# Optimization experiments

Measured on AMD Instinct MI355X. Metric: run time of the kernel, lower is better.

The kernel has to match this reference:

```python
import jax, jax.numpy as jnp
import numpy as np

N_NODES = 100000
N_EDGES = 1600000
INPUT_DIM = 128
HIDDEN = 128
OUTPUT_DIM = 2
NUM_LAYERS = 2
MAX_RECURSION = 10
TAU_THRESHOLD = 0.005


def setup_inputs() -> dict:
    key = jax.random.key(0)
    ks = jax.random.split(key, 16)
    s = 0.05
    x = jax.random.normal(ks[0], (N_NODES, INPUT_DIM), dtype=jnp.float32)
    edge_index = jax.random.randint(ks[1], (2, N_EDGES), 0, N_NODES, dtype=jnp.int64)
    W_in = jax.random.normal(ks[2], (HIDDEN, INPUT_DIM), dtype=jnp.float32) * s
    b_in = jax.random.normal(ks[3], (HIDDEN,), dtype=jnp.float32) * s
    Wd = jax.random.normal(ks[4], (NUM_LAYERS, HIDDEN, 2 * HIDDEN), dtype=jnp.float32) * s
    bd = jax.random.normal(ks[5], (NUM_LAYERS, HIDDEN), dtype=jnp.float32) * s
    Wt = jax.random.normal(ks[6], (1, HIDDEN), dtype=jnp.float32) * s
    bt = jax.random.normal(ks[7], (1,), dtype=jnp.float32) * s
    W_ih = jax.random.normal(ks[8], (3 * HIDDEN, HIDDEN), dtype=jnp.float32) * s
    W_hh = jax.random.normal(ks[9], (3 * HIDDEN, HIDDEN), dtype=jnp.float32) * s
    b_ih = jax.random.normal(ks[10], (3 * HIDDEN,), dtype=jnp.float32) * s
    b_hh = jax.random.normal(ks[11], (3 * HIDDEN,), dtype=jnp.float32) * s
    Wo = jax.random.normal(ks[12], (OUTPUT_DIM, HIDDEN), dtype=jnp.float32) * s
    bo = jax.random.normal(ks[13], (OUTPUT_DIM,), dtype=jnp.float32) * s
    return dict(x=x, edge_index=edge_index, W_in=W_in, b_in=b_in, Wd=Wd, bd=bd,
                Wt=Wt, bt=bt, W_ih=W_ih, W_hh=W_hh, b_ih=b_ih, b_hh=b_hh, Wo=Wo, bo=bo)


def _gru_cell(x, h, W_ih, W_hh, b_ih, b_hh):
    # torch.nn.GRUCell math
    gi = x @ W_ih.T + b_ih  # [N, 3H]
    gh = h @ W_hh.T + b_hh
    i_r, i_z, i_n = jnp.split(gi, 3, axis=-1)
    h_r, h_z, h_n = jnp.split(gh, 3, axis=-1)
    r = jax.nn.sigmoid(i_r + h_r)
    z = jax.nn.sigmoid(i_z + h_z)
    n = jnp.tanh(i_n + r * h_n)
    return (1.0 - z) * n + z * h


def reference(x, edge_index, W_in, b_in, Wd, bd, Wt, bt, W_ih, W_hh, b_ih, b_hh, Wo, bo):
    N = x.shape[0]
    row, col = edge_index[0], edge_index[1]
    h = jax.nn.relu(x @ W_in.T + b_in)  # [N, H]
    tau = None
    for l in range(NUM_LAYERS):
        diff = jnp.abs(h[row] - h[col])  # [E, H]
        diff_agg = jax.ops.segment_sum(diff, row, num_segments=N)  # [N, H]
        h = jax.nn.relu(jnp.concatenate([h, diff_agg], axis=-1) @ Wd[l].T + bd[l])
        tau = jax.nn.softplus(h @ Wt.T + bt).squeeze(-1)  # [N]
        # n_updates = clamp(floor(1/tau), max=MAX_RECURSION); node updated iff
        # n_updates > 0 and tau < TAU_THRESHOLD. The original inner loop applies
        # gru(diff_agg[i], h[i]) with the ORIGINAL h[i] each iteration, so repeated
        # application is idempotent -> single masked GRU step is exact same math.
        n_updates = jnp.minimum(jnp.floor(1.0 / tau).astype(jnp.int32), MAX_RECURSION)
        mask = (n_updates > 0) & (tau < TAU_THRESHOLD)
        h_gru = _gru_cell(diff_agg, h, W_ih, W_hh, b_ih, b_hh)
        h = jnp.where(mask[:, None], h_gru, h)
    out = h @ Wo.T + bo  # [N, OUTPUT_DIM]
    return out, tau
```

## Files before the change

kernel.cpp:

```cpp
#include <hip/hip_runtime.h>
#include <cstdint>
#include <cstddef>

#define HID 128
#define BSHIFT 7
#define NSB 256
#define MAXB 4096


__global__ __launch_bounds__(256)
void ecount_kernel(const int* __restrict__ row, int* __restrict__ countsT,
                   int E, int nbuck,
                   const float* __restrict__ W_in, const float* __restrict__ Wd,
                   const float* __restrict__ W_ih, const float* __restrict__ W_hh,
                   float* __restrict__ WinT, float* __restrict__ WdT0,
                   float* __restrict__ WdT1, float* __restrict__ WihT,
                   float* __restrict__ WhhT) {
  for (int i = blockIdx.x * 256 + threadIdx.x; i < 180224; i += NSB * 256) {
    int j = i;
    if (j < 16384) { int r = j >> 7, c = j & 127; WinT[c * 128 + r] = W_in[j]; continue; }
    j -= 16384;
    if (j < 32768) { int r = j >> 8, c = j & 255; WdT0[c * 128 + r] = Wd[j]; continue; }
    j -= 32768;
    if (j < 32768) { int r = j >> 8, c = j & 255; WdT1[c * 128 + r] = Wd[32768 + j]; continue; }
    j -= 32768;
    if (j < 49152) { int r = j >> 7, c = j & 127; WihT[c * 384 + r] = W_ih[j]; continue; }
    j -= 49152;
    { int r = j >> 7, c = j & 127; WhhT[c * 384 + r] = W_hh[j]; }
  }
  __shared__ int lh[1024];
  int b = blockIdx.x;
  for (int i = threadIdx.x; i < nbuck; i += 256) lh[i] = 0;
  __syncthreads();
  int per = (E + NSB - 1) / NSB;
  int s = b * per, e = min(s + per, E);
  for (int i = s + (int)threadIdx.x; i < e; i += 256)
    atomicAdd(&lh[row[i] >> BSHIFT], 1);
  __syncthreads();
  for (int i = threadIdx.x; i < nbuck; i += 256) countsT[i * NSB + b] = lh[i];
}

__global__ __launch_bounds__(NSB)
void bprefix_kernel(int* __restrict__ countsT, int* __restrict__ btotal, int nbuck) {
  __shared__ int sd[NSB];
  int bk = blockIdx.x;
  int t = threadIdx.x;
  int v = countsT[bk * NSB + t];
  sd[t] = v;
  __syncthreads();
  for (int off = 1; off < NSB; off <<= 1) {
    int u = (t >= off) ? sd[t - off] : 0;
    __syncthreads();
    sd[t] += u;
    __syncthreads();
  }
  countsT[bk * NSB + t] = sd[t] - v;
  if (t == NSB - 1) btotal[bk] = sd[t];
}

__global__ __launch_bounds__(1024)
void bstart_kernel(const int* __restrict__ btotal, int* __restrict__ bstart,
                   int* __restrict__ offsets, int N, int nbuck) {
  __shared__ int sd[1024];
  int t = threadIdx.x;
  int v = (t < nbuck) ? btotal[t] : 0;
  sd[t] = v;
  __syncthreads();
  for (int off = 1; off < 1024; off <<= 1) {
    int u = (t >= off) ? sd[t - off] : 0;
    __syncthreads();
    sd[t] += u;
    __syncthreads();
  }
  if (t < nbuck) bstart[t] = sd[t] - v;
  if (t == nbuck - 1) { bstart[nbuck] = sd[t]; offsets[N] = sd[t]; }
}

__global__ __launch_bounds__(256)
void escatter_kernel(const int* __restrict__ row, const int* __restrict__ col,
                     const int* __restrict__ countsT, const int* __restrict__ bstart,
                     int2* __restrict__ ebuf, int E, int nbuck) {
  __shared__ int lcur[1024];
  int b = blockIdx.x;
  for (int i = threadIdx.x; i < nbuck; i += 256)
    lcur[i] = bstart[i] + countsT[i * NSB + b];
  __syncthreads();
  int per = (E + NSB - 1) / NSB;
  int s = b * per, e = min(s + per, E);
  for (int i = s + (int)threadIdx.x; i < e; i += 256) {
    int r = row[i], c = col[i];
    int pos = atomicAdd(&lcur[r >> BSHIFT], 1);
    ebuf[pos] = make_int2(r, c);
  }
}

__global__ __launch_bounds__(256, 6)
void bsort_gin_kernel(const int2* __restrict__ ebuf, const int* __restrict__ bstart,
                      int* __restrict__ offsets, int* __restrict__ csr_col,
                      int N, int nbuck,
                      const float* __restrict__ A, const float* __restrict__ BT,
                      const float* __restrict__ bias, float* __restrict__ C, int G) {
  __shared__ union {
    struct { int cnt[128]; int off[128]; int cur[128]; int lcol[MAXB]; } s;
    struct { float As[32][68]; float Bs[32][128]; } g;
  } sm;
  int bid = blockIdx.x;
  int tid = threadIdx.x;
  if (bid < nbuck) {
    int bk = bid;
    int s = bstart[bk], e = bstart[bk + 1];
    int m = e - s;
    if (tid < 128) sm.s.cnt[tid] = 0;
    __syncthreads();
    for (int i = s + tid; i < e; i += 256)
      atomicAdd(&sm.s.cnt[ebuf[i].x & 127], 1);
    __syncthreads();
    if (tid < 128) sm.s.off[tid] = sm.s.cnt[tid];
    __syncthreads();
    for (int d = 1; d < 128; d <<= 1) {
      int v = 0;
      if (tid < 128 && tid >= d) v = sm.s.off[tid - d];
      __syncthreads();
      if (tid < 128) sm.s.off[tid] += v;
      __syncthreads();
    }
    if (tid < 128) {
      sm.s.cur[tid] = sm.s.off[tid] - sm.s.cnt[tid];
      int node = (bk << BSHIFT) + tid;
      if (node < N) offsets[node] = s + sm.s.off[tid] - sm.s.cnt[tid];
    }
    __syncthreads();
    if (m <= MAXB) {
      for (int i = s + tid; i < e; i += 256) {
        int2 rc = ebuf[i];
        int pos = atomicAdd(&sm.s.cur[rc.x & 127], 1);
        sm.s.lcol[pos] = rc.y;
      }
      __syncthreads();
      if (tid < 128) {
        int b0 = sm.s.off[tid] - sm.s.cnt[tid], b1 = sm.s.off[tid];
        for (int i = b0 + 1; i < b1; ++i) {
          int key = sm.s.lcol[i];
          int j = i - 1;
          while (j >= b0 && sm.s.lcol[j] > key) { sm.s.lcol[j + 1] = sm.s.lcol[j]; --j; }
          sm.s.lcol[j + 1] = key;
        }
      }
      __syncthreads();
      for (int i = tid; i < m; i += 256) csr_col[s + i] = sm.s.lcol[i];
    } else {
      for (int i = s + tid; i < e; i += 256) {
        int2 rc = ebuf[i];
        int pos = atomicAdd(&sm.s.cur[rc.x & 127], 1);
        csr_col[s + pos] = rc.y;
      }
    }
    return;
  }
  int tile = bid - nbuck;
  if (tile >= G) return;
  int tx = tid & 31;
  int ty = tid >> 5;
  int i0 = tile * 64;
  int M = N;
  float acc[8][4] = {};
  for (int kc = 0; kc < 4; ++kc) {
    int ksrc = kc * 32;
    #pragma unroll
    for (int q = 0; q < 2; ++q) {
      int f = q * 256 + tid;
      int i = f >> 3;
      int kq = (f & 7) << 2;
      int ig = i0 + i; if (ig >= M) ig = M - 1;
      float4 v = *(const float4*)(A + (size_t)ig * HID + ksrc + kq);
      sm.g.As[kq + 0][i] = v.x; sm.g.As[kq + 1][i] = v.y;
      sm.g.As[kq + 2][i] = v.z; sm.g.As[kq + 3][i] = v.w;
    }
    #pragma unroll
    for (int q = 0; q < 4; ++q) {
      int f = q * 256 + tid;
      int k = f >> 5; int c4 = (f & 31) << 2;
      *(float4*)&sm.g.Bs[k][c4] = *(const float4*)(BT + (size_t)(ksrc + k) * HID + c4);
    }
    __syncthreads();
    #pragma unroll
    for (int k = 0; k < 32; ++k) {
      float a[8];
      const float4* ap = (const float4*)&sm.g.As[k][ty * 8];
      float4 a0 = ap[0], a1 = ap[1];
      a[0]=a0.x; a[1]=a0.y; a[2]=a0.z; a[3]=a0.w;
      a[4]=a1.x; a[5]=a1.y; a[6]=a1.z; a[7]=a1.w;
      float4 b4 = *(const float4*)&sm.g.Bs[k][tx * 4];
      #pragma unroll
      for (int r = 0; r < 8; ++r) {
        acc[r][0] = fmaf(a[r], b4.x, acc[r][0]);
        acc[r][1] = fmaf(a[r], b4.y, acc[r][1]);
        acc[r][2] = fmaf(a[r], b4.z, acc[r][2]);
        acc[r][3] = fmaf(a[r], b4.w, acc[r][3]);
      }
    }
    __syncthreads();
  }
  float4 bias4 = *(const float4*)(bias + tx * 4);
  #pragma unroll
  for (int r = 0; r < 8; ++r) {
    int row = i0 + ty * 8 + r;
    if (row >= M) continue;
    float4 v4 = make_float4(fmaxf(acc[r][0] + bias4.x, 0.f),
                            fmaxf(acc[r][1] + bias4.y, 0.f),
                            fmaxf(acc[r][2] + bias4.z, 0.f),
                            fmaxf(acc[r][3] + bias4.w, 0.f));
    *(float4*)(C + (size_t)row * HID + tx * 4) = v4;
  }
}

__device__ __forceinline__ void agg_one_node(const float* __restrict__ h,
                                             const int* __restrict__ offsets,
                                             const int* __restrict__ csr_col,
                                             float* __restrict__ diff, int node) {
  int lane = threadIdx.x & 63;
  int start = offsets[node], end = offsets[node + 1];
  int deg = end - start;
  const float2* hrow = (const float2*)(h + (size_t)node * HID);
  float2 hv = hrow[lane];
  float a0 = 0.f, a1 = 0.f;

  int batch = min(deg, 64);
  int myc = (lane < batch) ? csr_col[start + lane] : 0;
  int j = 0;
  for (; j + 16 <= batch; j += 16) {
    const float2* p0 = (const float2*)(h + (size_t)__shfl(myc, j + 0) * HID);
    const float2* p1 = (const float2*)(h + (size_t)__shfl(myc, j + 1) * HID);
    const float2* p2 = (const float2*)(h + (size_t)__shfl(myc, j + 2) * HID);
    const float2* p3 = (const float2*)(h + (size_t)__shfl(myc, j + 3) * HID);
    const float2* p4 = (const float2*)(h + (size_t)__shfl(myc, j + 4) * HID);
    const float2* p5 = (const float2*)(h + (size_t)__shfl(myc, j + 5) * HID);
    const float2* p6 = (const float2*)(h + (size_t)__shfl(myc, j + 6) * HID);
    const float2* p7 = (const float2*)(h + (size_t)__shfl(myc, j + 7) * HID);
    const float2* q0 = (const float2*)(h + (size_t)__shfl(myc, j + 8) * HID);
    const float2* q1 = (const float2*)(h + (size_t)__shfl(myc, j + 9) * HID);
    const float2* q2 = (const float2*)(h + (size_t)__shfl(myc, j + 10) * HID);
    const float2* q3 = (const float2*)(h + (size_t)__shfl(myc, j + 11) * HID);
    const float2* q4 = (const float2*)(h + (size_t)__shfl(myc, j + 12) * HID);
    const float2* q5 = (const float2*)(h + (size_t)__shfl(myc, j + 13) * HID);
    const float2* q6 = (const float2*)(h + (size_t)__shfl(myc, j + 14) * HID);
    const float2* q7 = (const float2*)(h + (size_t)__shfl(myc, j + 15) * HID);
    float2 x0 = p0[lane], x1 = p1[lane], x2 = p2[lane], x3 = p3[lane];
    float2 x4 = p4[lane], x5 = p5[lane], x6 = p6[lane], x7 = p7[lane];
    float2 y0 = q0[lane], y1 = q1[lane], y2 = q2[lane], y3 = q3[lane];
    float2 y4 = q4[lane], y5 = q5[lane], y6 = q6[lane], y7 = q7[lane];
    a0 += fabsf(hv.x - x0.x) + fabsf(hv.x - x1.x) + fabsf(hv.x - x2.x) + fabsf(hv.x - x3.x)
        + fabsf(hv.x - x4.x) + fabsf(hv.x - x5.x) + fabsf(hv.x - x6.x) + fabsf(hv.x - x7.x);
    a1 += fabsf(hv.y - x0.y) + fabsf(hv.y - x1.y) + fabsf(hv.y - x2.y) + fabsf(hv.y - x3.y)
        + fabsf(hv.y - x4.y) + fabsf(hv.y - x5.y) + fabsf(hv.y - x6.y) + fabsf(hv.y - x7.y);
    a0 += fabsf(hv.x - y0.x) + fabsf(hv.x - y1.x) + fabsf(hv.x - y2.x) + fabsf(hv.x - y3.x)
        + fabsf(hv.x - y4.x) + fabsf(hv.x - y5.x) + fabsf(hv.x - y6.x) + fabsf(hv.x - y7.x);
    a1 += fabsf(hv.y - y0.y) + fabsf(hv.y - y1.y) + fabsf(hv.y - y2.y) + fabsf(hv.y - y3.y)
        + fabsf(hv.y - y4.y) + fabsf(hv.y - y5.y) + fabsf(hv.y - y6.y) + fabsf(hv.y - y7.y);
  }
  for (; j + 8 <= batch; j += 8) {
    const float2* p0 = (const float2*)(h + (size_t)__shfl(myc, j + 0) * HID);
    const float2* p1 = (const float2*)(h + (size_t)__shfl(myc, j + 1) * HID);
    const float2* p2 = (const float2*)(h + (size_t)__shfl(myc, j + 2) * HID);
    const float2* p3 = (const float2*)(h + (size_t)__shfl(myc, j + 3) * HID);
    const float2* p4 = (const float2*)(h + (size_t)__shfl(myc, j + 4) * HID);
    const float2* p5 = (const float2*)(h + (size_t)__shfl(myc, j + 5) * HID);
    const float2* p6 = (const float2*)(h + (size_t)__shfl(myc, j + 6) * HID);
    const float2* p7 = (const float2*)(h + (size_t)__shfl(myc, j + 7) * HID);
    float2 x0 = p0[lane], x1 = p1[lane], x2 = p2[lane], x3 = p3[lane];
    float2 x4 = p4[lane], x5 = p5[lane], x6 = p6[lane], x7 = p7[lane];
    a0 += fabsf(hv.x - x0.x) + fabsf(hv.x - x1.x) + fabsf(hv.x - x2.x) + fabsf(hv.x - x3.x)
        + fabsf(hv.x - x4.x) + fabsf(hv.x - x5.x) + fabsf(hv.x - x6.x) + fabsf(hv.x - x7.x);
    a1 += fabsf(hv.y - x0.y) + fabsf(hv.y - x1.y) + fabsf(hv.y - x2.y) + fabsf(hv.y - x3.y)
        + fabsf(hv.y - x4.y) + fabsf(hv.y - x5.y) + fabsf(hv.y - x6.y) + fabsf(hv.y - x7.y);
  }
  for (; j < batch; ++j) {
    const float2* p = (const float2*)(h + (size_t)__shfl(myc, j) * HID);
    float2 x = p[lane];
    a0 += fabsf(hv.x - x.x);
    a1 += fabsf(hv.y - x.y);
  }
  for (int e = start + 64; e < end; ++e) {
    const float2* p = (const float2*)(h + (size_t)csr_col[e] * HID);
    float2 x = p[lane];
    a0 += fabsf(hv.x - x.x);
    a1 += fabsf(hv.y - x.y);
  }
  *(float2*)(diff + (size_t)node * HID + 2 * lane) = make_float2(a0, a1);
}

__global__ __launch_bounds__(256, 6)
void fused_ap1_kernel(const float* __restrict__ h, const int* __restrict__ offsets,
                      const int* __restrict__ csr_col, float* __restrict__ diff,
                      const float* __restrict__ BT, float* __restrict__ Cpart,
                      int M, int G) {
  __shared__ float As[32][68];
  __shared__ float Bs[32][128];
  int bid = blockIdx.x;
  int tid = threadIdx.x;
  int q17 = bid / 17, r17 = bid % 17;
  if (r17 == 0 && q17 < G) {
    int tx = tid & 31;
    int ty = tid >> 5;
    int i0 = q17 * 64;
    float acc[8][4] = {};
    for (int kc = 0; kc < 4; ++kc) {
      int ksrc = kc * 32;
      #pragma unroll
      for (int q = 0; q < 2; ++q) {
        int f = q * 256 + tid;
        int i = f >> 3;
        int kq = (f & 7) << 2;
        int ig = i0 + i; if (ig >= M) ig = M - 1;
        float4 v = *(const float4*)(h + (size_t)ig * HID + ksrc + kq);
        As[kq + 0][i] = v.x; As[kq + 1][i] = v.y;
        As[kq + 2][i] = v.z; As[kq + 3][i] = v.w;
      }
      #pragma unroll
      for (int q = 0; q < 4; ++q) {
        int f = q * 256 + tid;
        int k = f >> 5; int c4 = (f & 31) << 2;
        *(float4*)&Bs[k][c4] = *(const float4*)(BT + (size_t)(ksrc + k) * HID + c4);
      }
      __syncthreads();
      #pragma unroll
      for (int k = 0; k < 32; ++k) {
        float a[8];
        const float4* ap = (const float4*)&As[k][ty * 8];
        float4 a0 = ap[0], a1 = ap[1];
        a[0]=a0.x; a[1]=a0.y; a[2]=a0.z; a[3]=a0.w;
        a[4]=a1.x; a[5]=a1.y; a[6]=a1.z; a[7]=a1.w;
        float4 b4 = *(const float4*)&Bs[k][tx * 4];
        #pragma unroll
        for (int r = 0; r < 8; ++r) {
          acc[r][0] = fmaf(a[r], b4.x, acc[r][0]);
          acc[r][1] = fmaf(a[r], b4.y, acc[r][1]);
          acc[r][2] = fmaf(a[r], b4.z, acc[r][2]);
          acc[r][3] = fmaf(a[r], b4.w, acc[r][3]);
        }
      }
      __syncthreads();
    }
    #pragma unroll
    for (int r = 0; r < 8; ++r) {
      int row = i0 + ty * 8 + r;
      if (row < M) {
        *(float4*)(Cpart + (size_t)row * HID + tx * 4) =
            make_float4(acc[r][0], acc[r][1], acc[r][2], acc[r][3]);
      }
    }
  } else {
    int ngemm_before = (bid + 16) / 17; if (ngemm_before > G) ngemm_before = G;
    int aidx = bid - ngemm_before;
    int wave = tid >> 6;
    int node = aidx * 4 + wave;
    if (node >= M) return;
    agg_one_node(h, offsets, csr_col, diff, node);
  }
}

template<bool OUT>
__global__ __launch_bounds__(256)
void gemm_p2_kernel(const float* __restrict__ A2, const float* __restrict__ BT,
                    const float* __restrict__ bias, float* __restrict__ C,
                    int M,
                    const float* __restrict__ Wt, const float* __restrict__ bt,
                    float* __restrict__ tau_out,
                    const float* __restrict__ WihT, const float* __restrict__ WhhT,
                    const float* __restrict__ b_ih, const float* __restrict__ b_hh,
                    const float* __restrict__ Wo, const float* __restrict__ bo,
                    float* __restrict__ outp) {
  __shared__ float As[32][68];
  __shared__ float Bs[32][128];
  __shared__ float taured[64];
  __shared__ float dl_s[HID];
  __shared__ float hl_s[HID];
  __shared__ int mrows[64];
  __shared__ int mcnt_s;
  __shared__ float osum_s[2][2];
  int tid = threadIdx.x;
  int tx = tid & 31;
  int ty = tid >> 5;
  int i0 = blockIdx.x * 64;
  if (tid == 0) mcnt_s = 0;
  float acc[8][4] = {};
  #pragma unroll
  for (int r = 0; r < 8; ++r) {
    int row = i0 + ty * 8 + r;
    if (row < M) {
      float4 v = *(const float4*)(C + (size_t)row * HID + tx * 4);
      acc[r][0] = v.x; acc[r][1] = v.y; acc[r][2] = v.z; acc[r][3] = v.w;
    }
  }
  for (int kc = 4; kc < 8; ++kc) {
    int ksrc = (kc & 3) * 32;
    int kglob = kc * 32;
    #pragma unroll
    for (int q = 0; q < 2; ++q) {
      int f = q * 256 + tid;
      int i = f >> 3;
      int kq = (f & 7) << 2;
      int ig = i0 + i; if (ig >= M) ig = M - 1;
      float4 v = *(const float4*)(A2 + (size_t)ig * HID + ksrc + kq);
      As[kq + 0][i] = v.x; As[kq + 1][i] = v.y;
      As[kq + 2][i] = v.z; As[kq + 3][i] = v.w;
    }
    #pragma unroll
    for (int q = 0; q < 4; ++q) {
      int f = q * 256 + tid;
      int k = f >> 5; int c4 = (f & 31) << 2;
      *(float4*)&Bs[k][c4] = *(const float4*)(BT + (size_t)(kglob + k) * HID + c4);
    }
    __syncthreads();
    #pragma unroll
    for (int k = 0; k < 32; ++k) {
      float a[8];
      const float4* ap = (const float4*)&As[k][ty * 8];
      float4 a0 = ap[0], a1 = ap[1];
      a[0]=a0.x; a[1]=a0.y; a[2]=a0.z; a[3]=a0.w;
      a[4]=a1.x; a[5]=a1.y; a[6]=a1.z; a[7]=a1.w;
      float4 b4 = *(const float4*)&Bs[k][tx * 4];
      #pragma unroll
      for (int r = 0; r < 8; ++r) {
        acc[r][0] = fmaf(a[r], b4.x, acc[r][0]);
        acc[r][1] = fmaf(a[r], b4.y, acc[r][1]);
        acc[r][2] = fmaf(a[r], b4.z, acc[r][2]);
        acc[r][3] = fmaf(a[r], b4.w, acc[r][3]);
      }
    }
    __syncthreads();
  }

  float4 bias4 = *(const float4*)(bias + tx * 4);
  float bias_r[4] = {bias4.x, bias4.y, bias4.z, bias4.w};
  float4 w4 = *(const float4*)(Wt + tx * 4);
  float wt_r[4] = {w4.x, w4.y, w4.z, w4.w};
  float4 wo0 = make_float4(0.f, 0.f, 0.f, 0.f);
  float4 wo1 = make_float4(0.f, 0.f, 0.f, 0.f);
  if constexpr (OUT) {
    wo0 = *(const float4*)(Wo + tx * 4);
    wo1 = *(const float4*)(Wo + 128 + tx * 4);
  }
  #pragma unroll
  for (int r = 0; r < 8; ++r) {
    int row = i0 + ty * 8 + r;
    bool ok = row < M;
    float v0 = fmaxf(acc[r][0] + bias_r[0], 0.f);
    float v1 = fmaxf(acc[r][1] + bias_r[1], 0.f);
    float v2 = fmaxf(acc[r][2] + bias_r[2], 0.f);
    float v3 = fmaxf(acc[r][3] + bias_r[3], 0.f);
    if (ok) {
      float4 v4 = make_float4(v0, v1, v2, v3);
      *(float4*)(C + (size_t)row * HID + tx * 4) = v4;
    }
    if constexpr (OUT) {
      float o0 = v0 * wo0.x + v1 * wo0.y + v2 * wo0.z + v3 * wo0.w;
      float o1 = v0 * wo1.x + v1 * wo1.y + v2 * wo1.z + v3 * wo1.w;
      o0 += __shfl_down(o0, 16, 32); o1 += __shfl_down(o1, 16, 32);
      o0 += __shfl_down(o0, 8, 32);  o1 += __shfl_down(o1, 8, 32);
      o0 += __shfl_down(o0, 4, 32);  o1 += __shfl_down(o1, 4, 32);
      o0 += __shfl_down(o0, 2, 32);  o1 += __shfl_down(o1, 2, 32);
      o0 += __shfl_down(o0, 1, 32);  o1 += __shfl_down(o1, 1, 32);
      if (tx == 0 && ok) {
        outp[(size_t)row * 2 + 0] = o0 + bo[0];
        outp[(size_t)row * 2 + 1] = o1 + bo[1];
      }
    }
    {
      float pf = v0 * wt_r[0];
      pf = fmaf(v1, wt_r[1], pf);
      pf = fmaf(v2, wt_r[2], pf);
      pf = fmaf(v3, wt_r[3], pf);
      pf += __shfl_down(pf, 16, 32);
      pf += __shfl_down(pf, 8, 32);
      pf += __shfl_down(pf, 4, 32);
      pf += __shfl_down(pf, 2, 32);
      pf += __shfl_down(pf, 1, 32);
      if (tx == 0) taured[ty * 8 + r] = pf;
    }
  }
  __syncthreads();
  if (tid < 64) {
    int row = i0 + tid;
    if (row < M) {
      float pre = taured[tid] + bt[0];
      float tau = (pre > 20.f) ? pre : log1pf(expf(pre));
      tau_out[row] = tau;
      if (tau < 0.005f && (1.0f / tau) < 2147483648.0f) {
        int pos = atomicAdd(&mcnt_s, 1);
        mrows[pos] = tid;
      }
    }
  }
  __syncthreads();
  int mc = mcnt_s;
  for (int mi = 0; mi < mc; ++mi) {
    int lrow = mrows[mi];
    int grow = i0 + lrow;
    if (tid < 128) {
      dl_s[tid] = A2[(size_t)grow * HID + tid];
      hl_s[tid] = C[(size_t)grow * HID + tid];
    }
    __syncthreads();
    if (tid < 128) {
      int txg = tid;
      float air = 0.f, aiz = 0.f, ain_ = 0.f, ahr = 0.f, ahz = 0.f, ahn = 0.f;
      for (int k = 0; k < HID; ++k) {
        float wir = WihT[k * 384 + txg];
        float wiz = WihT[k * 384 + 128 + txg];
        float win = WihT[k * 384 + 256 + txg];
        float whr = WhhT[k * 384 + txg];
        float whz = WhhT[k * 384 + 128 + txg];
        float whn = WhhT[k * 384 + 256 + txg];
        float dk = dl_s[k];
        float hk = hl_s[k];
        air = fmaf(dk, wir, air);
        aiz = fmaf(dk, wiz, aiz);
        ain_ = fmaf(dk, win, ain_);
        ahr = fmaf(hk, whr, ahr);
        ahz = fmaf(hk, whz, ahz);
        ahn = fmaf(hk, whn, ahn);
      }
      float bir = b_ih[txg], biz = b_ih[128 + txg], bin = b_ih[256 + txg];
      float bhr = b_hh[txg], bhz = b_hh[128 + txg], bhn = b_hh[256 + txg];
      float rg = 1.f / (1.f + expf(-((air + bir) + (ahr + bhr))));
      float z  = 1.f / (1.f + expf(-((aiz + biz) + (ahz + bhz))));
      float n  = tanhf((ain_ + bin) + rg * (ahn + bhn));
      float hv = hl_s[txg];
      float hnew = (1.f - z) * n + z * hv;
      C[(size_t)grow * HID + txg] = hnew;
      if constexpr (OUT) {
        float p0 = hnew * Wo[txg];
        float p1 = hnew * Wo[128 + txg];
        p0 += __shfl_down(p0, 32, 64); p1 += __shfl_down(p1, 32, 64);
        p0 += __shfl_down(p0, 16, 64); p1 += __shfl_down(p1, 16, 64);
        p0 += __shfl_down(p0, 8, 64);  p1 += __shfl_down(p1, 8, 64);
        p0 += __shfl_down(p0, 4, 64);  p1 += __shfl_down(p1, 4, 64);
        p0 += __shfl_down(p0, 2, 64);  p1 += __shfl_down(p1, 2, 64);
        p0 += __shfl_down(p0, 1, 64);  p1 += __shfl_down(p1, 1, 64);
        if ((txg & 63) == 0) {
          osum_s[txg >> 6][0] = p0;
          osum_s[txg >> 6][1] = p1;
        }
      }
    }
    __syncthreads();
    if constexpr (OUT) {
      if (tid == 0) {
        outp[(size_t)grow * 2 + 0] = osum_s[0][0] + osum_s[1][0] + bo[0];
        outp[(size_t)grow * 2 + 1] = osum_s[0][1] + osum_s[1][1] + bo[1];
      }
    }
  }
}

extern "C" void kernel_launch(void* const* d_in, const int* in_sizes, int n_in,
                              void* d_out, int out_size, void* d_ws, size_t ws_size,
                              hipStream_t stream) {
  const float* x    = (const float*)d_in[0];
  const int*   ei   = (const int*)d_in[1];
  const float* W_in = (const float*)d_in[2];
  const float* b_in = (const float*)d_in[3];
  const float* Wd   = (const float*)d_in[4];
  const float* bd   = (const float*)d_in[5];
  const float* Wt   = (const float*)d_in[6];
  const float* bt   = (const float*)d_in[7];
  const float* W_ih = (const float*)d_in[8];
  const float* W_hh = (const float*)d_in[9];
  const float* b_ih = (const float*)d_in[10];
  const float* b_hh = (const float*)d_in[11];
  const float* Wo   = (const float*)d_in[12];
  const float* bo   = (const float*)d_in[13];

  const int N = in_sizes[0] / HID;
  const int E = in_sizes[1] / 2;
  const int* rowp = ei;
  const int* colp = ei + E;
  const int nbuck = (N + (1 << BSHIFT) - 1) >> BSHIFT;

  char* p = (char*)d_ws;
  auto alloc = [&](size_t bytes) { void* r = (void*)p; p += (bytes + 255) & ~(size_t)255; return r; };
  float* hA     = (float*)alloc((size_t)N * HID * 4);
  float* hB     = (float*)alloc((size_t)N * HID * 4);
  float* diff   = (float*)alloc((size_t)N * HID * 4);
  float* WinT   = (float*)alloc(128 * 128 * 4);
  float* WdT0   = (float*)alloc(256 * 128 * 4);
  float* WdT1   = (float*)alloc(256 * 128 * 4);
  float* WihT   = (float*)alloc(128 * 384 * 4);
  float* WhhT   = (float*)alloc(128 * 384 * 4);
  float* tau0   = (float*)alloc((size_t)N * 4);
  int*   countsT= (int*)alloc((size_t)1024 * NSB * 4);
  int*   btotal = (int*)alloc(1024 * 4);
  int*   bstart = (int*)alloc(1028 * 4);
  int*   offs   = (int*)alloc(((size_t)N + 1) * 4);
  int*   csrcol = (int*)alloc((size_t)E * 4);
  int2*  ebuf   = (int2*)alloc((size_t)E * 8);

  float* out_ptr = (float*)d_out;
  float* tau_out = (float*)d_out + (size_t)N * 2;

  ecount_kernel<<<NSB, 256, 0, stream>>>(rowp, countsT, E, nbuck,
                                         W_in, Wd, W_ih, W_hh,
                                         WinT, WdT0, WdT1, WihT, WhhT);
  bprefix_kernel<<<nbuck, NSB, 0, stream>>>(countsT, btotal, nbuck);
  bstart_kernel<<<1, 1024, 0, stream>>>(btotal, bstart, offs, N, nbuck);
  escatter_kernel<<<NSB, 256, 0, stream>>>(rowp, colp, countsT, bstart, ebuf, E, nbuck);

  const int G = (N + 63) / 64;
  const int agg_groups = (N + 3) / 4;
  const int fused_blocks = G + agg_groups;

  bsort_gin_kernel<<<nbuck + G, 256, 0, stream>>>(
      ebuf, bstart, offs, csrcol, N, nbuck, x, WinT, b_in, hA, G);

  fused_ap1_kernel<<<fused_blocks, 256, 0, stream>>>(
      hA, offs, csrcol, diff, WdT0, hB, N, G);
  gemm_p2_kernel<false><<<G, 256, 0, stream>>>(
      diff, WdT0, bd, hB, N, Wt, bt, tau0,
      WihT, WhhT, b_ih, b_hh, nullptr, nullptr, nullptr);

  fused_ap1_kernel<<<fused_blocks, 256, 0, stream>>>(
      hB, offs, csrcol, diff, WdT1, hA, N, G);
  gemm_p2_kernel<true><<<G, 256, 0, stream>>>(
      diff, WdT1, bd + 128, hA, N, Wt, bt, tau_out,
      WihT, WhhT, b_ih, b_hh, Wo, bo, out_ptr);
}
```

Baseline: 662.4 us.

## Split aggregation into halves and overlap second-phase GEMM with second-half aggregation

Each layer's edge aggregation is now split across two launches. The first launch aggregates the first half of the nodes alongside all first-phase GEMM tiles. The second launch aggregates the remaining nodes while running the second-phase GEMM and GRU epilogue for the first-half tiles, whose diff rows are already complete. A final launch finishes the second-phase tiles for the second half. This aims to hide the dependent GEMM/GRU work behind memory-bound gather work, at the cost of an extra launch and a lower occupancy bound on the fused kernel.

```diff
diff --git a/kernel.cpp b/kernel.cpp
--- a/kernel.cpp
+++ b/kernel.cpp
@@ -293,16 +293,17 @@
 void fused_ap1_kernel(const float* __restrict__ h, const int* __restrict__ offsets,
                       const int* __restrict__ csr_col, float* __restrict__ diff,
                       const float* __restrict__ BT, float* __restrict__ Cpart,
-                      int M, int G) {
+                      int M, int G, int node_base, int nagg) {
   __shared__ float As[32][68];
   __shared__ float Bs[32][128];
   int bid = blockIdx.x;
   int tid = threadIdx.x;
-  int q17 = bid / 17, r17 = bid % 17;
-  if (r17 == 0 && q17 < G) {
+  const int R = 9;
+  int qg = bid / R, rg = bid % R;
+  if (rg == 0 && qg < G) {
     int tx = tid & 31;
     int ty = tid >> 5;
-    int i0 = q17 * 64;
+    int i0 = qg * 64;
     float acc[8][4] = {};
     for (int kc = 0; kc < 4; ++kc) {
       int ksrc = kc * 32;
@@ -350,26 +351,26 @@
       }
     }
   } else {
-    int ngemm_before = (bid + 16) / 17; if (ngemm_before > G) ngemm_before = G;
+    int ngemm_before = (bid + R - 1) / R; if (ngemm_before > G) ngemm_before = G;
     int aidx = bid - ngemm_before;
+    if (aidx >= nagg) return;
     int wave = tid >> 6;
-    int node = aidx * 4 + wave;
+    int node = node_base + aidx * 4 + wave;
     if (node >= M) return;
     agg_one_node(h, offsets, csr_col, diff, node);
   }
 }
 
 template<bool OUT>
-__global__ __launch_bounds__(256)
-void gemm_p2_kernel(const float* __restrict__ A2, const float* __restrict__ BT,
-                    const float* __restrict__ bias, float* __restrict__ C,
-                    int M,
-                    const float* __restrict__ Wt, const float* __restrict__ bt,
-                    float* __restrict__ tau_out,
-                    const float* __restrict__ WihT, const float* __restrict__ WhhT,
-                    const float* __restrict__ b_ih, const float* __restrict__ b_hh,
-                    const float* __restrict__ Wo, const float* __restrict__ bo,
-                    float* __restrict__ outp) {
+__device__ __forceinline__
+void p2_body(int tile, const float* __restrict__ A2, const float* __restrict__ BT,
+             const float* __restrict__ bias, float* __restrict__ C, int M,
+             const float* __restrict__ Wt, const float* __restrict__ bt,
+             float* __restrict__ tau_out,
+             const float* __restrict__ WihT, const float* __restrict__ WhhT,
+             const float* __restrict__ b_ih, const float* __restrict__ b_hh,
+             const float* __restrict__ Wo, const float* __restrict__ bo,
+             float* __restrict__ outp) {
   __shared__ float As[32][68];
   __shared__ float Bs[32][128];
   __shared__ float taured[64];
@@ -381,7 +382,7 @@
   int tid = threadIdx.x;
   int tx = tid & 31;
   int ty = tid >> 5;
-  int i0 = blockIdx.x * 64;
+  int i0 = tile * 64;
   if (tid == 0) mcnt_s = 0;
   float acc[8][4] = {};
   #pragma unroll
@@ -554,6 +555,50 @@
   }
 }
 
+template<bool OUT>
+__global__ __launch_bounds__(256, 4)
+void fused_ap2_kernel(const float* __restrict__ h, const int* __restrict__ offsets,
+                      const int* __restrict__ csr_col, float* __restrict__ diff,
+                      const float* __restrict__ BT, const float* __restrict__ bias,
+                      float* __restrict__ C, int M, int node_base, int nagg, int TH,
+                      const float* __restrict__ Wt, const float* __restrict__ bt,
+                      float* __restrict__ tau_out,
+                      const float* __restrict__ WihT, const float* __restrict__ WhhT,
+                      const float* __restrict__ b_ih, const float* __restrict__ b_hh,
+                      const float* __restrict__ Wo, const float* __restrict__ bo,
+                      float* __restrict__ outp) {
+  int bid = blockIdx.x;
+  int tid = threadIdx.x;
+  const int R = 17;
+  int qg = bid / R, rg = bid % R;
+  if (rg == 0 && qg < TH) {
+    p2_body<OUT>(qg, diff, BT, bias, C, M, Wt, bt, tau_out,
+                 WihT, WhhT, b_ih, b_hh, Wo, bo, outp);
+  } else {
+    int ngemm_before = (bid + R - 1) / R; if (ngemm_before > TH) ngemm_before = TH;
+    int aidx = bid - ngemm_before;
+    if (aidx >= nagg) return;
+    int wave = tid >> 6;
+    int node = node_base + aidx * 4 + wave;
+    if (node >= M) return;
+    agg_one_node(h, offsets, csr_col, diff, node);
+  }
+}
+
+template<bool OUT>
+__global__ __launch_bounds__(256)
+void gemm_p2_kernel(int toff, const float* __restrict__ A2, const float* __restrict__ BT,
+                    const float* __restrict__ bias, float* __restrict__ C, int M,
+                    const float* __restrict__ Wt, const float* __restrict__ bt,
+                    float* __restrict__ tau_out,
+                    const float* __restrict__ WihT, const float* __restrict__ WhhT,
+                    const float* __restrict__ b_ih, const float* __restrict__ b_hh,
+                    const float* __restrict__ Wo, const float* __restrict__ bo,
+                    float* __restrict__ outp) {
+  p2_body<OUT>(blockIdx.x + toff, A2, BT, bias, C, M, Wt, bt, tau_out,
+               WihT, WhhT, b_ih, b_hh, Wo, bo, outp);
+}
+
 extern "C" void kernel_launch(void* const* d_in, const int* in_sizes, int n_in,
                               void* d_out, int out_size, void* d_ws, size_t ws_size,
                               hipStream_t stream) {
@@ -606,22 +651,33 @@
   bstart_kernel<<<1, 1024, 0, stream>>>(btotal, bstart, offs, N, nbuck);
   escatter_kernel<<<NSB, 256, 0, stream>>>(rowp, colp, countsT, bstart, ebuf, E, nbuck);
 
-  const int G = (N + 63) / 64;
-  const int agg_groups = (N + 3) / 4;
-  const int fused_blocks = G + agg_groups;
+  const int G  = (N + 63) / 64;
+  const int TH = G / 2;
+  const int NH = TH * 64;
+  const int NAGG1 = NH / 4;
+  const int NAGG2 = (N - NH + 3) / 4;
+  const int K1_blocks = NAGG1 + G;
+  const int K2_blocks = NAGG2 + TH;
+  const int TR = G - TH;
 
   bsort_gin_kernel<<<nbuck + G, 256, 0, stream>>>(
       ebuf, bstart, offs, csrcol, N, nbuck, x, WinT, b_in, hA, G);
 
-  fused_ap1_kernel<<<fused_blocks, 256, 0, stream>>>(
-      hA, offs, csrcol, diff, WdT0, hB, N, G);
-  gemm_p2_kernel<false><<<G, 256, 0, stream>>>(
-      diff, WdT0, bd, hB, N, Wt, bt, tau0,
+  fused_ap1_kernel<<<K1_blocks, 256, 0, stream>>>(
+      hA, offs, csrcol, diff, WdT0, hB, N, G, 0, NAGG1);
+  fused_ap2_kernel<false><<<K2_blocks, 256, 0, stream>>>(
+      hA, offs, csrcol, diff, WdT0, bd, hB, N, NH, NAGG2, TH,
+      Wt, bt, tau0, WihT, WhhT, b_ih, b_hh, nullptr, nullptr, nullptr);
+  gemm_p2_kernel<false><<<TR, 256, 0, stream>>>(
+      TH, diff, WdT0, bd, hB, N, Wt, bt, tau0,
       WihT, WhhT, b_ih, b_hh, nullptr, nullptr, nullptr);
 
-  fused_ap1_kernel<<<fused_blocks, 256, 0, stream>>>(
-      hB, offs, csrcol, diff, WdT1, hA, N, G);
-  gemm_p2_kernel<true><<<G, 256, 0, stream>>>(
-      diff, WdT1, bd + 128, hA, N, Wt, bt, tau_out,
+  fused_ap1_kernel<<<K1_blocks, 256, 0, stream>>>(
+      hB, offs, csrcol, diff, WdT1, hA, N, G, 0, NAGG1);
+  fused_ap2_kernel<true><<<K2_blocks, 256, 0, stream>>>(
+      hB, offs, csrcol, diff, WdT1, bd + 128, hA, N, NH, NAGG2, TH,
+      Wt, bt, tau_out, WihT, WhhT, b_ih, b_hh, Wo, bo, out_ptr);
+  gemm_p2_kernel<true><<<TR, 256, 0, stream>>>(
+      TH, diff, WdT1, bd + 128, hA, N, Wt, bt, tau_out,
       WihT, WhhT, b_ih, b_hh, Wo, bo, out_ptr);
 }
```

Result: slower. 703.0 us (+6.1%).
